# Kernel optimization log

Measured on AMD Instinct MI355X. Metric: run time of the kernel, lower is better.

## Reference

```python
import jax, jax.numpy as jnp
import numpy as np

B = 1_000_000          # number of 2-node graphs
N = 2 * B              # total nodes
IN_D, HID_D, OUT_D = 4, 16, 4


def setup_inputs() -> dict:
    key = jax.random.key(0)
    ks = jax.random.split(key, 5)
    x = jax.random.normal(ks[0], (N, IN_D), dtype=jnp.float32)
    # per-graph bidirectional edges (0->1, 1->0) offset by 2*graph_id,
    # mirroring edge_index + offsets.repeat_interleave(2)
    off = jnp.arange(B, dtype=jnp.int64) * 2
    src = jnp.stack([off, off + 1], axis=1).reshape(-1)      # [2B]
    dst = jnp.stack([off + 1, off], axis=1).reshape(-1)      # [2B]
    edge_index = jnp.stack([src, dst], axis=0)               # [2, 2B]
    s = 1.0 / np.sqrt(IN_D)
    W_root1 = jax.random.uniform(ks[1], (IN_D, HID_D), jnp.float32, -s, s)
    W_rel1 = jax.random.uniform(ks[2], (IN_D, HID_D), jnp.float32, -s, s)
    b1 = jnp.zeros((HID_D,), jnp.float32)
    s2 = 1.0 / np.sqrt(HID_D)
    W_root2 = jax.random.uniform(ks[3], (HID_D, OUT_D), jnp.float32, -s2, s2)
    W_rel2 = jax.random.uniform(ks[4], (HID_D, OUT_D), jnp.float32, -s2, s2)
    b2 = jnp.zeros((OUT_D,), jnp.float32)
    return {"x": x, "edge_index": edge_index, "W_root1": W_root1,
            "W_rel1": W_rel1, "b1": b1, "W_root2": W_root2,
            "W_rel2": W_rel2, "b2": b2}


def _graph_conv(x, src, dst, W_root, W_rel, b):
    # GraphConv: out_i = x_i @ W_root + (sum_{j->i} x_j) @ W_rel + b
    agg = jax.ops.segment_sum(x[src], dst, num_segments=N)
    return x @ W_root + agg @ W_rel + b


def reference(x, edge_index, W_root1, W_rel1, b1, W_root2, W_rel2, b2):
    src, dst = edge_index[0], edge_index[1]
    h = jax.nn.relu(_graph_conv(x, src, dst, W_root1, W_rel1, b1))
    out = _graph_conv(h, src, dst, W_root2, W_rel2, b2)
    return out
```

## Files before the change

### kernel.cpp

```cpp
#include <hip/hip_runtime.h>


__global__ void __launch_bounds__(256) gnn2_kernel(
    const float* __restrict__ x,
    const float* __restrict__ Wr1, const float* __restrict__ We1,
    const float* __restrict__ b1,
    const float* __restrict__ Wr2, const float* __restrict__ We2,
    const float* __restrict__ b2,
    float* __restrict__ out, int nGraphs)
{
    __shared__ float4 sWh1[16], sWm1[16], sWh2[16], sWm2[16];
    __shared__ float  sB1[16], sB2[4];

    const int tid = threadIdx.x;
    if (tid < 64) {
        const int k = tid >> 2, d = tid & 3;
        const float r = Wr1[d * 16 + k], e = We1[d * 16 + k];
        ((float*)sWh1)[tid] = 0.5f * (r + e);
        ((float*)sWm1)[tid] = 0.5f * (r - e);
    } else if (tid < 128) {
        const int t = tid - 64;
        const int j = t >> 4, k = t & 15;
        const float r = Wr2[k * 4 + j], e = We2[k * 4 + j];
        ((float*)sWh2)[t] = 0.5f * (r + e);
        ((float*)sWm2)[t] = 0.5f * (r - e);
    } else if (tid < 144) {
        sB1[tid - 128] = b1[tid - 128];
    } else if (tid < 148) {
        sB2[tid - 144] = b2[tid - 144];
    }
    __syncthreads();

    const float4* __restrict__ xv = (const float4*)x;
    float4* __restrict__ ov = (float4*)out;

    int g = blockIdx.x * blockDim.x + threadIdx.x;
    const int stride = gridDim.x * blockDim.x;
    for (; g < nGraphs; g += stride) {
        const float4 a = xv[2 * g];
        const float4 c = xv[2 * g + 1];

        float4 s, d;
        s.x = a.x + c.x; s.y = a.y + c.y; s.z = a.z + c.z; s.w = a.w + c.w;
        d.x = a.x - c.x; d.y = a.y - c.y; d.z = a.z - c.z; d.w = a.w - c.w;

        float s2[16], d2[16];
        #pragma unroll
        for (int k = 0; k < 16; ++k) {
            const float4 wh = sWh1[k];
            const float4 wm = sWm1[k];
            const float u = fmaf(s.x, wh.x, fmaf(s.y, wh.y, fmaf(s.z, wh.z, s.w * wh.w)));
            const float v = fmaf(d.x, wm.x, fmaf(d.y, wm.y, fmaf(d.z, wm.z, d.w * wm.w)));
            const float bb = sB1[k];
            const float h0 = fmaxf(u + v + bb, 0.0f);
            const float h1 = fmaxf(u - v + bb, 0.0f);
            s2[k] = h0 + h1;
            d2[k] = h0 - h1;
        }

        float o0[4], o1[4];
        #pragma unroll
        for (int j = 0; j < 4; ++j) {
            float au = 0.0f, av = 0.0f;
            #pragma unroll
            for (int q = 0; q < 4; ++q) {
                const float4 wh = sWh2[j * 4 + q];
                const float4 wm = sWm2[j * 4 + q];
                au = fmaf(s2[4 * q + 0], wh.x, au);
                au = fmaf(s2[4 * q + 1], wh.y, au);
                au = fmaf(s2[4 * q + 2], wh.z, au);
                au = fmaf(s2[4 * q + 3], wh.w, au);
                av = fmaf(d2[4 * q + 0], wm.x, av);
                av = fmaf(d2[4 * q + 1], wm.y, av);
                av = fmaf(d2[4 * q + 2], wm.z, av);
                av = fmaf(d2[4 * q + 3], wm.w, av);
            }
            const float bb = sB2[j];
            o0[j] = au + av + bb;
            o1[j] = au - av + bb;
        }

        ov[2 * g]     = make_float4(o0[0], o0[1], o0[2], o0[3]);
        ov[2 * g + 1] = make_float4(o1[0], o1[1], o1[2], o1[3]);
    }
}

extern "C" void kernel_launch(void* const* d_in, const int* in_sizes, int n_in,
                              void* d_out, int out_size, void* d_ws, size_t ws_size,
                              hipStream_t stream) {
    const float* x   = (const float*)d_in[0];
    const float* Wr1 = (const float*)d_in[2];
    const float* We1 = (const float*)d_in[3];
    const float* b1  = (const float*)d_in[4];
    const float* Wr2 = (const float*)d_in[5];
    const float* We2 = (const float*)d_in[6];
    const float* b2  = (const float*)d_in[7];
    float* out = (float*)d_out;

    const int nGraphs = in_sizes[0] / 8;

    const int block = 256;
    const int grid = 2048;
    gnn2_kernel<<<grid, block, 0, stream>>>(x, Wr1, We1, b1, Wr2, We2, b2,
                                            out, nGraphs);
}
```

Before: 118.9 us.

## Drop shared-memory weights, use one thread per graph with nontemporal stores

Removes the shared-memory staging of the folded weights and the block-wide barrier. Each thread now handles exactly one graph and reads the weights directly from global memory as uniform scalar loads. The grid-stride loop is replaced by a full-size grid, and the outputs are written with nontemporal stores to reduce cache pollution. The sum/difference algebra is also dropped in favour of the direct root/rel formulation, which roughly doubles the FMA count per graph. The win depends on scalar-cache broadcast and the memory-bound streaming outweighing the extra arithmetic.

```diff
diff --git a/kernel.cpp b/kernel.cpp
--- a/kernel.cpp
+++ b/kernel.cpp
@@ -1,88 +1,79 @@
 #include <hip/hip_runtime.h>
 
 
+typedef float f4 __attribute__((ext_vector_type(4)));
+
 __global__ void __launch_bounds__(256) gnn2_kernel(
-    const float* __restrict__ x,
+    const f4* __restrict__ xv,
     const float* __restrict__ Wr1, const float* __restrict__ We1,
     const float* __restrict__ b1,
     const float* __restrict__ Wr2, const float* __restrict__ We2,
     const float* __restrict__ b2,
-    float* __restrict__ out, int nGraphs)
+    f4* __restrict__ ov, int nGraphs)
 {
-    __shared__ float4 sWh1[16], sWm1[16], sWh2[16], sWm2[16];
-    __shared__ float  sB1[16], sB2[4];
+    const int g = blockIdx.x * blockDim.x + threadIdx.x;
+    if (g >= nGraphs) return;
 
-    const int tid = threadIdx.x;
-    if (tid < 64) {
-        const int k = tid >> 2, d = tid & 3;
-        const float r = Wr1[d * 16 + k], e = We1[d * 16 + k];
-        ((float*)sWh1)[tid] = 0.5f * (r + e);
-        ((float*)sWm1)[tid] = 0.5f * (r - e);
-    } else if (tid < 128) {
-        const int t = tid - 64;
-        const int j = t >> 4, k = t & 15;
-        const float r = Wr2[k * 4 + j], e = We2[k * 4 + j];
-        ((float*)sWh2)[t] = 0.5f * (r + e);
-        ((float*)sWm2)[t] = 0.5f * (r - e);
-    } else if (tid < 144) {
-        sB1[tid - 128] = b1[tid - 128];
-    } else if (tid < 148) {
-        sB2[tid - 144] = b2[tid - 144];
+    const f4 a = xv[2 * g];
+    const f4 c = xv[2 * g + 1];
+
+    float h0[16], h1[16];
+#pragma unroll
+    for (int k = 0; k < 16; ++k) {
+        const float wr_0 = Wr1[0 * 16 + k];
+        const float wr_1 = Wr1[1 * 16 + k];
+        const float wr_2 = Wr1[2 * 16 + k];
+        const float wr_3 = Wr1[3 * 16 + k];
+        const float we_0 = We1[0 * 16 + k];
+        const float we_1 = We1[1 * 16 + k];
+        const float we_2 = We1[2 * 16 + k];
+        const float we_3 = We1[3 * 16 + k];
+        const float bb = b1[k];
+
+        float t0 = bb;
+        t0 = fmaf(a.x, wr_0, t0);
+        t0 = fmaf(a.y, wr_1, t0);
+        t0 = fmaf(a.z, wr_2, t0);
+        t0 = fmaf(a.w, wr_3, t0);
+        t0 = fmaf(c.x, we_0, t0);
+        t0 = fmaf(c.y, we_1, t0);
+        t0 = fmaf(c.z, we_2, t0);
+        t0 = fmaf(c.w, we_3, t0);
+
+        float t1 = bb;
+        t1 = fmaf(c.x, wr_0, t1);
+        t1 = fmaf(c.y, wr_1, t1);
+        t1 = fmaf(c.z, wr_2, t1);
+        t1 = fmaf(c.w, wr_3, t1);
+        t1 = fmaf(a.x, we_0, t1);
+        t1 = fmaf(a.y, we_1, t1);
+        t1 = fmaf(a.z, we_2, t1);
+        t1 = fmaf(a.w, we_3, t1);
+
+        h0[k] = fmaxf(t0, 0.0f);
+        h1[k] = fmaxf(t1, 0.0f);
     }
-    __syncthreads();
 
-    const float4* __restrict__ xv = (const float4*)x;
-    float4* __restrict__ ov = (float4*)out;
+    f4 o0, o1;
+#pragma unroll
+    for (int j = 0; j < 4; ++j) {
+        const float bb = b2[j];
+        float s0 = bb, s1 = bb;
+#pragma unroll
+        for (int k = 0; k < 16; ++k) {
+            const float wr = Wr2[k * 4 + j];
+            const float we = We2[k * 4 + j];
+            s0 = fmaf(h0[k], wr, s0);
+            s0 = fmaf(h1[k], we, s0);
+            s1 = fmaf(h1[k], wr, s1);
+            s1 = fmaf(h0[k], we, s1);
+        }
+        o0[j] = s0;
+        o1[j] = s1;
+    }
 
-    int g = blockIdx.x * blockDim.x + threadIdx.x;
-    const int stride = gridDim.x * blockDim.x;
-    for (; g < nGraphs; g += stride) {
-        const float4 a = xv[2 * g];
-        const float4 c = xv[2 * g + 1];
-
-        float4 s, d;
-        s.x = a.x + c.x; s.y = a.y + c.y; s.z = a.z + c.z; s.w = a.w + c.w;
-        d.x = a.x - c.x; d.y = a.y - c.y; d.z = a.z - c.z; d.w = a.w - c.w;
-
-        float s2[16], d2[16];
-        #pragma unroll
-        for (int k = 0; k < 16; ++k) {
-            const float4 wh = sWh1[k];
-            const float4 wm = sWm1[k];
-            const float u = fmaf(s.x, wh.x, fmaf(s.y, wh.y, fmaf(s.z, wh.z, s.w * wh.w)));
-            const float v = fmaf(d.x, wm.x, fmaf(d.y, wm.y, fmaf(d.z, wm.z, d.w * wm.w)));
-            const float bb = sB1[k];
-            const float h0 = fmaxf(u + v + bb, 0.0f);
-            const float h1 = fmaxf(u - v + bb, 0.0f);
-            s2[k] = h0 + h1;
-            d2[k] = h0 - h1;
-        }
-
-        float o0[4], o1[4];
-        #pragma unroll
-        for (int j = 0; j < 4; ++j) {
-            float au = 0.0f, av = 0.0f;
-            #pragma unroll
-            for (int q = 0; q < 4; ++q) {
-                const float4 wh = sWh2[j * 4 + q];
-                const float4 wm = sWm2[j * 4 + q];
-                au = fmaf(s2[4 * q + 0], wh.x, au);
-                au = fmaf(s2[4 * q + 1], wh.y, au);
-                au = fmaf(s2[4 * q + 2], wh.z, au);
-                au = fmaf(s2[4 * q + 3], wh.w, au);
-                av = fmaf(d2[4 * q + 0], wm.x, av);
-                av = fmaf(d2[4 * q + 1], wm.y, av);
-                av = fmaf(d2[4 * q + 2], wm.z, av);
-                av = fmaf(d2[4 * q + 3], wm.w, av);
-            }
-            const float bb = sB2[j];
-            o0[j] = au + av + bb;
-            o1[j] = au - av + bb;
-        }
-
-        ov[2 * g]     = make_float4(o0[0], o0[1], o0[2], o0[3]);
-        ov[2 * g + 1] = make_float4(o1[0], o1[1], o1[2], o1[3]);
-    }
+    __builtin_nontemporal_store(o0, &ov[2 * g]);
+    __builtin_nontemporal_store(o1, &ov[2 * g + 1]);
 }
 
 extern "C" void kernel_launch(void* const* d_in, const int* in_sizes, int n_in,
@@ -95,12 +86,11 @@
     const float* Wr2 = (const float*)d_in[5];
     const float* We2 = (const float*)d_in[6];
     const float* b2  = (const float*)d_in[7];
-    float* out = (float*)d_out;
 
     const int nGraphs = in_sizes[0] / 8;
 
     const int block = 256;
-    const int grid = 2048;
-    gnn2_kernel<<<grid, block, 0, stream>>>(x, Wr1, We1, b1, Wr2, We2, b2,
-                                            out, nGraphs);
+    const int grid  = (nGraphs + block - 1) / block;
+    gnn2_kernel<<<grid, block, 0, stream>>>((const f4*)x, Wr1, We1, b1,
+                                            Wr2, We2, b2, (f4*)d_out, nGraphs);
 }
```

Result: faster. 104.5 us (-12.1%).
